# Kernel optimization log

Hardware: AMD Instinct MI355X
Metric: run time of the kernel (lower is better)

The kernel has to match this reference:

```python
import jax, jax.numpy as jnp
import numpy as np

N_NODES = 50000   # nodes per (single) node type
N_EDGES = 1000000 # edges per edge type (avg degree ~20)
IN_SIZE = 256
OUT_SIZE = 128
N_ETYPES = 3


def setup_inputs() -> dict:
    key = jax.random.key(0)
    k0, k1, k2, k3, k4 = jax.random.split(key, 5)
    x = jax.random.normal(k0, (N_NODES, IN_SIZE), jnp.float32)
    edge_src = jax.random.randint(k1, (N_ETYPES, N_EDGES), 0, N_NODES, jnp.int32)
    edge_dst = jax.random.randint(k2, (N_ETYPES, N_EDGES), 0, N_NODES, jnp.int32)
    # per-etype Linear params (weight stored as [in, out] so Wh = x @ W + b)
    W = jax.random.normal(k3, (N_ETYPES, IN_SIZE, OUT_SIZE), jnp.float32) / np.sqrt(IN_SIZE).astype(np.float32)
    b = jax.random.normal(k4, (N_ETYPES, OUT_SIZE), jnp.float32) * 0.01
    return {"x": x, "edge_src": edge_src, "edge_dst": edge_dst, "W": W, "b": b}


def reference(x, edge_src, edge_dst, W, b):
    # Per-etype linear projection: Wh[e] = x @ W[e] + b[e]  -> [E_types, N, OUT]
    Wh = jnp.einsum('ni,eio->eno', x, W) + b[:, None, :]

    def agg_one(wh, src, dst):
        # copy_u: gather projected src features along edges  [N_EDGES, OUT]
        msgs = wh[src]
        # mean reduce onto dst nodes (scatter-mean); zero for nodes w/o in-edges
        sums = jax.ops.segment_sum(msgs, dst, num_segments=N_NODES)
        deg = jax.ops.segment_sum(jnp.ones((N_EDGES,), wh.dtype), dst, num_segments=N_NODES)
        return jnp.where(deg[:, None] > 0, sums / jnp.maximum(deg, 1.0)[:, None], 0.0)

    h = jax.vmap(agg_one)(Wh, edge_src, edge_dst)  # [E_types, N, OUT]
    # agg='stack' cross-type reducer -> [N, E_types, OUT]
    return jnp.transpose(h, (1, 0, 2))
```

## Files before the change

### kernel.cpp

```cpp
#include <hip/hip_runtime.h>

#define N_NODES 50000
#define N_EDGES 1000000
#define N_ETYPES 3
#define NB 782
#define TOTB (N_ETYPES * NB)
#define EPB 8192
#define EPT 32
#define FB  ((N_EDGES + EPB - 1) / EPB)
#define GCAP 2048

typedef _Float16 f16x8 __attribute__((ext_vector_type(8)));
typedef float f32x4 __attribute__((ext_vector_type(4)));

__global__ void k_prep(const float* __restrict__ x, _Float16* __restrict__ x16,
                       const float* __restrict__ W, _Float16* __restrict__ Wt) {
    int bid = blockIdx.x;
    if (bid < 6250) {
        int id = bid * 256 + threadIdx.x;
        const float* p = x + (size_t)id * 8;
        f32x4 lo = *(const f32x4*)p;
        f32x4 hi = *(const f32x4*)(p + 4);
        f16x8 v;
        #pragma unroll
        for (int j = 0; j < 4; ++j) {
            v[j]     = (_Float16)lo[j];
            v[j + 4] = (_Float16)hi[j];
        }
        *(f16x8*)(x16 + (size_t)id * 8) = v;
    } else {
        int id = (bid - 6250) * 256 + threadIdx.x;
        int e   = id >> 15;
        int rem = id & 32767;
        int k   = rem >> 7;
        int n   = rem & 127;
        Wt[(size_t)e * 32768 + (size_t)n * 256 + k] =
            (_Float16)W[(size_t)e * 32768 + (size_t)k * 128 + n];
    }
}

__global__ __launch_bounds__(256) void k_gemm(
    const _Float16* __restrict__ x16,
    const _Float16* __restrict__ Wt,
    const float* __restrict__ b,
    unsigned short* __restrict__ Wh)
{
    const int e    = blockIdx.y;
    const int tid  = threadIdx.x;
    const int lane = tid & 63;
    const int w    = tid >> 6;
    const int q    = lane >> 4;
    const int c    = lane & 15;
    const int rowBase = blockIdx.x * 128;
    const _Float16* Bt = Wt + (size_t)e * 32768;

    f32x4 acc[2][8];
    #pragma unroll
    for (int mt = 0; mt < 2; ++mt)
        #pragma unroll
        for (int nt = 0; nt < 8; ++nt)
            acc[mt][nt] = (f32x4){0.f, 0.f, 0.f, 0.f};

    int arow[2];
    #pragma unroll
    for (int mt = 0; mt < 2; ++mt) {
        int r = rowBase + w * 32 + mt * 16 + c;
        arow[mt] = (r < N_NODES) ? r : (N_NODES - 1);
    }

    #pragma unroll
    for (int ks = 0; ks < 8; ++ks) {
        f16x8 afrag[2];
        #pragma unroll
        for (int mt = 0; mt < 2; ++mt)
            afrag[mt] = *(const f16x8*)(x16 + (size_t)arow[mt] * 256 + ks * 32 + q * 8);
        #pragma unroll
        for (int nt = 0; nt < 8; ++nt) {
            f16x8 bfrag = *(const f16x8*)(Bt + (size_t)(nt * 16 + c) * 256 + ks * 32 + q * 8);
            #pragma unroll
            for (int mt = 0; mt < 2; ++mt)
                acc[mt][nt] = __builtin_amdgcn_mfma_f32_16x16x32_f16(
                    afrag[mt], bfrag, acc[mt][nt], 0, 0, 0);
        }
    }

    const size_t whBase = (size_t)e * N_NODES * 128;
    #pragma unroll
    for (int nt = 0; nt < 8; ++nt) {
        float bias = b[e * 128 + nt * 16 + c];
        #pragma unroll
        for (int mt = 0; mt < 2; ++mt) {
            int baseRow = rowBase + w * 32 + mt * 16 + q * 4;
            #pragma unroll
            for (int r = 0; r < 4; ++r) {
                int row = baseRow + r;
                if (row < N_NODES) {
                    float v = acc[mt][nt][r] + bias;
                    Wh[whBase + (size_t)row * 128 + nt * 16 + c] =
                        __builtin_bit_cast(unsigned short, (_Float16)v);
                }
            }
        }
    }
}

__global__ __launch_bounds__(256) void k_fill_b(
    const int* __restrict__ src, const int* __restrict__ dst,
    int* __restrict__ gcur, unsigned* __restrict__ grec)
{
    __shared__ int lcnt[NB];
    __shared__ int lbase[NB];
    const int e   = blockIdx.y;
    const int tid = threadIdx.x;
    const int beg = blockIdx.x * EPB;
    const int* se = src + (size_t)e * N_EDGES;
    const int* de = dst + (size_t)e * N_EDGES;

    for (int j = tid; j < NB; j += 256) lcnt[j] = 0;
    __syncthreads();

    unsigned rec[EPT];
    int      bl [EPT];
    #pragma unroll
    for (int k = 0; k < EPT; ++k) {
        int i = beg + k * 256 + tid;
        if (i < N_EDGES) {
            int s = __builtin_nontemporal_load(se + i);
            int d = __builtin_nontemporal_load(de + i);
            int b = d >> 6;
            int lpos = atomicAdd(&lcnt[b], 1);
            rec[k] = (unsigned)s | ((unsigned)(d & 63) << 16);
            bl[k]  = b | (lpos << 10);
        } else {
            bl[k] = -1;
        }
    }
    __syncthreads();
    for (int j = tid; j < NB; j += 256) {
        int c = lcnt[j];
        lbase[j] = c ? atomicAdd(&gcur[e * NB + j], c) : 0;
    }
    __syncthreads();
    #pragma unroll
    for (int k = 0; k < EPT; ++k) {
        if (bl[k] >= 0) {
            int b    = bl[k] & 1023;
            int pos  = lbase[b] + (bl[k] >> 10);
            if (pos < GCAP)
                grec[(size_t)(e * NB + b) * GCAP + pos] = rec[k];
        }
    }
}

__global__ __launch_bounds__(256) void k_bagg(
    const int* __restrict__ cnt_b, const unsigned* __restrict__ grec,
    const unsigned short* __restrict__ Wh, float* __restrict__ out)
{
    __shared__ unsigned       rec_s[GCAP];
    __shared__ unsigned short nbr_s[GCAP];
    __shared__ int ndeg[64], ncur[64], nstart[64];
    const int e    = blockIdx.y;
    const int bx   = blockIdx.x;
    const int tid  = threadIdx.x;
    const int lane = tid & 63;
    const int w    = tid >> 6;
    const int half = lane >> 5;
    const int sub  = lane & 31;
    const int eb   = e * NB + bx;
    const size_t beg = (size_t)eb * GCAP;
    int m = cnt_b[eb];
    if (m > GCAP) m = GCAP;
    const unsigned* base = (const unsigned*)Wh + (size_t)e * N_NODES * 64;

    if (tid < 64) ndeg[tid] = 0;
    __syncthreads();

    for (int i = tid; i < m; i += 256) {
        unsigned r = __builtin_nontemporal_load(grec + beg + i);
        rec_s[i] = r;
        atomicAdd(&ndeg[r >> 16], 1);
    }
    __syncthreads();
    if (tid < 64) {
        int v = ndeg[tid];
        int s = v;
        #pragma unroll
        for (int d = 1; d < 64; d <<= 1) {
            int t = __shfl_up(s, d);
            if (tid >= d) s += t;
        }
        int excl = s - v;
        nstart[tid] = excl;
        ncur[tid]   = excl;
    }
    __syncthreads();
    for (int i = tid; i < m; i += 256) {
        unsigned r = rec_s[i];
        int p = atomicAdd(&ncur[r >> 16], 1);
        nbr_s[p] = (unsigned short)(r & 0xFFFFu);
    }
    __syncthreads();

    for (int t = 0; t < 16; ++t) {
        int node = w * 16 + t;
        int st = nstart[node];
        int dg = ndeg[node];
        float a0 = 0.f, a1 = 0.f, a2 = 0.f, a3 = 0.f;
        for (int c0 = 0; c0 < dg; c0 += 64) {
            int mm = dg - c0; if (mm > 64) mm = 64;
            int idx = (c0 + lane < dg) ? (int)nbr_s[st + c0 + lane] : 0;
            int fullp = mm >> 1;
            int p = 0;
            for (; p + 8 <= fullp; p += 8) {
                uint2 u[8];
                #pragma unroll
                for (int k = 0; k < 8; ++k) {
                    int r0 = 2 * (p + k);
                    int s0 = __builtin_amdgcn_readlane(idx, r0);
                    int s1 = __builtin_amdgcn_readlane(idx, r0 + 1);
                    int s  = half ? s1 : s0;
                    u[k] = *(const uint2*)(base + (size_t)s * 64 + (sub << 1));
                }
                #pragma unroll
                for (int k = 0; k < 8; ++k) {
                    a0 += (float)__builtin_bit_cast(_Float16, (unsigned short)(u[k].x & 0xFFFFu));
                    a1 += (float)__builtin_bit_cast(_Float16, (unsigned short)(u[k].x >> 16));
                    a2 += (float)__builtin_bit_cast(_Float16, (unsigned short)(u[k].y & 0xFFFFu));
                    a3 += (float)__builtin_bit_cast(_Float16, (unsigned short)(u[k].y >> 16));
                }
            }
            if (2 * p < mm) {
                uint2 u[8];
                #pragma unroll
                for (int k = 0; k < 8; ++k) {
                    int r0 = 2 * (p + k);
                    int r0c = (r0     < mm) ? r0     : 0;
                    int r1c = (r0 + 1 < mm) ? r0 + 1 : 0;
                    int s0 = __builtin_amdgcn_readlane(idx, r0c);
                    int s1 = __builtin_amdgcn_readlane(idx, r1c);
                    int s  = half ? s1 : s0;
                    u[k] = *(const uint2*)(base + (size_t)s * 64 + (sub << 1));
                }
                #pragma unroll
                for (int k = 0; k < 8; ++k) {
                    if (2 * (p + k) + half < mm) {
                        a0 += (float)__builtin_bit_cast(_Float16, (unsigned short)(u[k].x & 0xFFFFu));
                        a1 += (float)__builtin_bit_cast(_Float16, (unsigned short)(u[k].x >> 16));
                        a2 += (float)__builtin_bit_cast(_Float16, (unsigned short)(u[k].y & 0xFFFFu));
                        a3 += (float)__builtin_bit_cast(_Float16, (unsigned short)(u[k].y >> 16));
                    }
                }
            }
        }
        a0 += __shfl_xor(a0, 32);
        a1 += __shfl_xor(a1, 32);
        a2 += __shfl_xor(a2, 32);
        a3 += __shfl_xor(a3, 32);
        int n = bx * 64 + node;
        if (half == 0 && n < N_NODES) {
            float inv = (dg > 0) ? (1.0f / (float)dg) : 0.f;
            f32x4 o = {a0 * inv, a1 * inv, a2 * inv, a3 * inv};
            __builtin_nontemporal_store(o, (f32x4*)(out + (size_t)n * 384 + e * 128 + (sub << 2)));
        }
    }
}

extern "C" void kernel_launch(void* const* d_in, const int* in_sizes, int n_in,
                              void* d_out, int out_size, void* d_ws, size_t ws_size,
                              hipStream_t stream) {
    const float* x    = (const float*)d_in[0];
    const int*   esrc = (const int*)d_in[1];
    const int*   edst = (const int*)d_in[2];
    const float* W    = (const float*)d_in[3];
    const float* bias = (const float*)d_in[4];
    float*       out  = (float*)d_out;

    char* ws = (char*)d_ws;
    _Float16*       Wt  = (_Float16*)ws;
    _Float16*       x16 = (_Float16*)(ws + 196608);
    unsigned short* Wh  = (unsigned short*)(ws + 25796608);
    unsigned* grec = (unsigned*)(ws + 64196608);
    int* gcur      = (int*)(ws + 83415040);

    hipMemsetAsync(gcur, 0, TOTB * sizeof(int), stream);

    k_prep<<<6250 + 384, 256, 0, stream>>>(x, x16, W, Wt);
    k_gemm<<<dim3(391, 3), 256, 0, stream>>>(x16, Wt, bias, Wh);
    k_fill_b<<<dim3(FB, 3), 256, 0, stream>>>(esrc, edst, gcur, grec);
    k_bagg<<<dim3(NB, 3), 256, 0, stream>>>(gcur, grec, Wh, out);
}
```

Measured before the change: 354.0 us.

## Fuse fp16 cast of x into GEMM and restructure edge bucketing into two passes

Removes the separate pass that converts x to fp16. The GEMM now loads fp32 x directly and converts it in registers, which saves writing and re-reading a 25MB intermediate buffer. The edge bucketing kernel becomes a two-pass count-then-scatter with four times more edges per block, so it needs fewer blocks and no per-thread register arrays, at the cost of reading dst twice. The GEMM is also reordered to run after the fill, and the GEMM now reads twice as many bytes for the A operand, which it loads three times (once per etype).

```diff
diff --git a/kernel.cpp b/kernel.cpp
--- a/kernel.cpp
+++ b/kernel.cpp
@@ -5,42 +5,24 @@
 #define N_ETYPES 3
 #define NB 782
 #define TOTB (N_ETYPES * NB)
-#define EPB 8192
-#define EPT 32
+#define EPB 32768
 #define FB  ((N_EDGES + EPB - 1) / EPB)
 #define GCAP 2048
 
 typedef _Float16 f16x8 __attribute__((ext_vector_type(8)));
 typedef float f32x4 __attribute__((ext_vector_type(4)));
 
-__global__ void k_prep(const float* __restrict__ x, _Float16* __restrict__ x16,
-                       const float* __restrict__ W, _Float16* __restrict__ Wt) {
-    int bid = blockIdx.x;
-    if (bid < 6250) {
-        int id = bid * 256 + threadIdx.x;
-        const float* p = x + (size_t)id * 8;
-        f32x4 lo = *(const f32x4*)p;
-        f32x4 hi = *(const f32x4*)(p + 4);
-        f16x8 v;
-        #pragma unroll
-        for (int j = 0; j < 4; ++j) {
-            v[j]     = (_Float16)lo[j];
-            v[j + 4] = (_Float16)hi[j];
-        }
-        *(f16x8*)(x16 + (size_t)id * 8) = v;
-    } else {
-        int id = (bid - 6250) * 256 + threadIdx.x;
-        int e   = id >> 15;
-        int rem = id & 32767;
-        int k   = rem >> 7;
-        int n   = rem & 127;
-        Wt[(size_t)e * 32768 + (size_t)n * 256 + k] =
-            (_Float16)W[(size_t)e * 32768 + (size_t)k * 128 + n];
-    }
+__global__ void k_prep_w(const float* __restrict__ W, _Float16* __restrict__ Wt) {
+    int e  = blockIdx.y;
+    int id = blockIdx.x * blockDim.x + threadIdx.x;
+    int k  = id >> 7;
+    int n  = id & 127;
+    Wt[(size_t)e * 32768 + (size_t)n * 256 + k] =
+        (_Float16)W[(size_t)e * 32768 + (size_t)k * 128 + n];
 }
 
 __global__ __launch_bounds__(256) void k_gemm(
-    const _Float16* __restrict__ x16,
+    const float* __restrict__ x,
     const _Float16* __restrict__ Wt,
     const float* __restrict__ b,
     unsigned short* __restrict__ Wh)
@@ -72,8 +54,18 @@
     for (int ks = 0; ks < 8; ++ks) {
         f16x8 afrag[2];
         #pragma unroll
-        for (int mt = 0; mt < 2; ++mt)
-            afrag[mt] = *(const f16x8*)(x16 + (size_t)arow[mt] * 256 + ks * 32 + q * 8);
+        for (int mt = 0; mt < 2; ++mt) {
+            const float* xp = x + (size_t)arow[mt] * 256 + ks * 32 + q * 8;
+            f32x4 lo = *(const f32x4*)xp;
+            f32x4 hi = *(const f32x4*)(xp + 4);
+            f16x8 af;
+            #pragma unroll
+            for (int j = 0; j < 4; ++j) {
+                af[j]     = (_Float16)lo[j];
+                af[j + 4] = (_Float16)hi[j];
+            }
+            afrag[mt] = af;
+        }
         #pragma unroll
         for (int nt = 0; nt < 8; ++nt) {
             f16x8 bfrag = *(const f16x8*)(Bt + (size_t)(nt * 16 + c) * 256 + ks * 32 + q * 8);
@@ -104,7 +96,7 @@
     }
 }
 
-__global__ __launch_bounds__(256) void k_fill_b(
+__global__ __launch_bounds__(256) void k_fill(
     const int* __restrict__ src, const int* __restrict__ dst,
     int* __restrict__ gcur, unsigned* __restrict__ grec)
 {
@@ -113,42 +105,32 @@
     const int e   = blockIdx.y;
     const int tid = threadIdx.x;
     const int beg = blockIdx.x * EPB;
+    int end = beg + EPB; if (end > N_EDGES) end = N_EDGES;
     const int* se = src + (size_t)e * N_EDGES;
     const int* de = dst + (size_t)e * N_EDGES;
 
     for (int j = tid; j < NB; j += 256) lcnt[j] = 0;
     __syncthreads();
-
-    unsigned rec[EPT];
-    int      bl [EPT];
-    #pragma unroll
-    for (int k = 0; k < EPT; ++k) {
-        int i = beg + k * 256 + tid;
-        if (i < N_EDGES) {
-            int s = __builtin_nontemporal_load(se + i);
-            int d = __builtin_nontemporal_load(de + i);
-            int b = d >> 6;
-            int lpos = atomicAdd(&lcnt[b], 1);
-            rec[k] = (unsigned)s | ((unsigned)(d & 63) << 16);
-            bl[k]  = b | (lpos << 10);
-        } else {
-            bl[k] = -1;
-        }
-    }
+    #pragma unroll 4
+    for (int i = beg + tid; i < end; i += 256)
+        atomicAdd(&lcnt[__builtin_nontemporal_load(de + i) >> 6], 1);
     __syncthreads();
     for (int j = tid; j < NB; j += 256) {
         int c = lcnt[j];
         lbase[j] = c ? atomicAdd(&gcur[e * NB + j], c) : 0;
-    }
-    __syncthreads();
-    #pragma unroll
-    for (int k = 0; k < EPT; ++k) {
-        if (bl[k] >= 0) {
-            int b    = bl[k] & 1023;
-            int pos  = lbase[b] + (bl[k] >> 10);
-            if (pos < GCAP)
-                grec[(size_t)(e * NB + b) * GCAP + pos] = rec[k];
-        }
+        lcnt[j] = 0;
+    }
+    __syncthreads();
+    #pragma unroll 4
+    for (int i = beg + tid; i < end; i += 256) {
+        int s = __builtin_nontemporal_load(se + i);
+        int d = __builtin_nontemporal_load(de + i);
+        int b = d >> 6;
+        int lpos = atomicAdd(&lcnt[b], 1);
+        int pos = lbase[b] + lpos;
+        if (pos < GCAP)
+            grec[(size_t)(e * NB + b) * GCAP + pos] =
+                (unsigned)s | ((unsigned)(d & 63) << 16);
     }
 }
 
@@ -277,15 +259,14 @@
 
     char* ws = (char*)d_ws;
     _Float16*       Wt  = (_Float16*)ws;
-    _Float16*       x16 = (_Float16*)(ws + 196608);
-    unsigned short* Wh  = (unsigned short*)(ws + 25796608);
-    unsigned* grec = (unsigned*)(ws + 64196608);
-    int* gcur      = (int*)(ws + 83415040);
+    unsigned short* Wh  = (unsigned short*)(ws + 196608);
+    unsigned* grec = (unsigned*)(ws + 38596608);
+    int* gcur      = (int*)(ws + 57815040);
 
     hipMemsetAsync(gcur, 0, TOTB * sizeof(int), stream);
 
-    k_prep<<<6250 + 384, 256, 0, stream>>>(x, x16, W, Wt);
-    k_gemm<<<dim3(391, 3), 256, 0, stream>>>(x16, Wt, bias, Wh);
-    k_fill_b<<<dim3(FB, 3), 256, 0, stream>>>(esrc, edst, gcur, grec);
+    k_prep_w<<<dim3(128, 3), 256, 0, stream>>>(W, Wt);
+    k_fill<<<dim3(FB, 3), 256, 0, stream>>>(esrc, edst, gcur, grec);
+    k_gemm<<<dim3(391, 3), 256, 0, stream>>>(x, Wt, bias, Wh);
     k_bagg<<<dim3(NB, 3), 256, 0, stream>>>(gcur, grec, Wh, out);
 }
```

Measured after the change: 473.4 us. +33.7%, slower.
